# Kernel optimization log

Hardware: AMD Instinct MI355X
Metric: run time of the kernel (lower is better)

## Reference

```python
import jax, jax.numpy as jnp
import numpy as np

PH, PL = 2, 4          # high-band / low-band patch sizes
EPS_LN = 1e-5          # torch LayerNorm eps
EPS_COS = 1e-8         # torch F.cosine_similarity eps


def _ln(x, w, b):
    m = x.mean(-1, keepdims=True)
    v = ((x - m) ** 2).mean(-1, keepdims=True)
    return (x - m) / jnp.sqrt(v + EPS_LN) * w + b


def setup_inputs() -> dict:
    key = jax.random.key(0)
    ks = jax.random.split(key, 8)
    B, Cb, Cs, H, W = 16, 256, 512, 128, 128
    hid = int(Cb * 2.0)  # token_expansion = 2.0 -> 512

    def n(k, shape, s=0.02):
        return jax.random.normal(k, shape, jnp.float32) * s

    return {
        "x_big": jax.random.normal(ks[0], (B, Cb, H, W), jnp.float32),
        "x_small": jax.random.normal(ks[1], (B, Cs, H // 2, W // 2), jnp.float32),
        # hf MLP: Linear(Cb->hid), LayerNorm(hid), Linear(hid->Cb); weights stored (in,out)
        "hf_w1": n(ks[2], (Cb, hid)), "hf_b1": jnp.zeros((hid,), jnp.float32),
        "hf_ln_w": jnp.ones((hid,), jnp.float32), "hf_ln_b": jnp.zeros((hid,), jnp.float32),
        "hf_w2": n(ks[3], (hid, Cb)), "hf_b2": jnp.zeros((Cb,), jnp.float32),
        "hf_prompt": jax.random.normal(ks[4], (Cb,), jnp.float32),
        # low_proj: 1x1 conv dim_small -> dim_big
        "low_w": n(ks[5], (Cs, Cb)), "low_b": jnp.zeros((Cb,), jnp.float32),
        # lf gate MLP
        "lf_w1": n(ks[6], (Cb, hid)), "lf_b1": jnp.zeros((hid,), jnp.float32),
        "lf_ln_w": jnp.ones((hid,), jnp.float32), "lf_ln_b": jnp.zeros((hid,), jnp.float32),
        "lf_w2": n(ks[7], (hid, Cb)), "lf_b2": jnp.zeros((Cb,), jnp.float32),
    }


def reference(x_big, x_small, hf_w1, hf_b1, hf_ln_w, hf_ln_b, hf_w2, hf_b2,
              hf_prompt, low_w, low_b, lf_w1, lf_b1, lf_ln_w, lf_ln_b, lf_w2, lf_b2):
    B, C, H, W = x_big.shape
    h2, w2 = H // 2, W // 2

    # --- forward Haar (depthwise 2x2 stride-2 conv, /4), expressed as 2x2 pixel combos ---
    xr = x_big.reshape(B, C, h2, 2, w2, 2)
    p00, p01 = xr[:, :, :, 0, :, 0], xr[:, :, :, 0, :, 1]
    p10, p11 = xr[:, :, :, 1, :, 0], xr[:, :, :, 1, :, 1]
    a = (p00 + p01 + p10 + p11) * 0.25
    hb = (p00 - p01 + p10 - p11) * 0.25
    vb = (p00 + p01 - p10 - p11) * 0.25
    db = (p00 - p01 - p10 + p11) * 0.25

    # --- high-band enhancement: per-patch |mean| token -> MLP -> cosine gate ---
    def enhance_high(band):
        hh, ww = h2 // PH, w2 // PH
        bp = band.reshape(B, C, hh, PH, ww, PH)
        # tokens z: (B, hh*ww, C) = mean |patch|
        z = jnp.abs(bp).mean(axis=(3, 5)).transpose(0, 2, 3, 1).reshape(B, hh * ww, C)
        q = _ln(z @ hf_w1 + hf_b1, hf_ln_w, hf_ln_b) @ hf_w2 + hf_b2
        dot = q @ hf_prompt
        nq = jnp.linalg.norm(q, axis=-1)
        npr = jnp.linalg.norm(hf_prompt)
        sim = dot / (jnp.maximum(nq, EPS_COS) * jnp.maximum(npr, EPS_COS))
        alpha = jax.nn.relu(sim).reshape(B, 1, hh, 1, ww, 1)
        return (bp * alpha).reshape(B, C, h2, w2)

    h_enh = enhance_high(hb)
    v_enh = enhance_high(vb)
    d_enh = enhance_high(db)

    # --- low-band enhancement: 1x1 proj guide -> per-patch mean token -> sigmoid gate ---
    guide = jnp.einsum('bshw,sd->bdhw', x_small, low_w) + low_b[None, :, None, None]
    hh, ww = h2 // PL, w2 // PL
    k_tok = guide.reshape(B, C, hh, PL, ww, PL).mean(axis=(3, 5))
    k_tok = k_tok.transpose(0, 2, 3, 1).reshape(B, hh * ww, C)
    gate = jax.nn.sigmoid(_ln(k_tok @ lf_w1 + lf_b1, lf_ln_w, lf_ln_b) @ lf_w2 + lf_b2)
    gate = gate.reshape(B, hh, ww, C).transpose(0, 3, 1, 2)  # (B, C, hh, ww)
    a_enh = (a.reshape(B, C, hh, PL, ww, PL) * gate[:, :, :, None, :, None]).reshape(B, C, h2, w2)

    # --- inverse Haar (conv_transpose with raw weights, no /4) ---
    o00 = a_enh + h_enh + v_enh + d_enh
    o01 = a_enh - h_enh + v_enh - d_enh
    o10 = a_enh + h_enh - v_enh - d_enh
    o11 = a_enh - h_enh - v_enh + d_enh
    top = jnp.stack([o00, o01], axis=-1)           # (B,C,h2,w2,2)
    bot = jnp.stack([o10, o11], axis=-1)
    return jnp.stack([top, bot], axis=3).reshape(B, C, H, W)
```

## Files before the change

### kernel.cpp

```cpp
#include <hip/hip_runtime.h>
#include <cstdint>
#include <cmath>

typedef unsigned short u16;
typedef __bf16 bf16x8 __attribute__((ext_vector_type(8)));
typedef float f32x4 __attribute__((ext_vector_type(4)));

__device__ __forceinline__ u16 bf16_rne(float v) {
    union { float f; uint32_t u; } a; a.f = v;
    uint32_t r = a.u + 0x7fffu + ((a.u >> 16) & 1u);
    return (u16)(r >> 16);
}
__device__ __forceinline__ float bf16_to_f(u16 h) {
    union { uint32_t u; float f; } a; a.u = ((uint32_t)h) << 16;
    return a.f;
}
__device__ __forceinline__ uint32_t pack_pair(float v0, float v1, uint32_t& lopack) {
    const u16 h0 = bf16_rne(v0), h1 = bf16_rne(v1);
    const u16 l0 = bf16_rne(v0 - bf16_to_f(h0)), l1 = bf16_rne(v1 - bf16_to_f(h1));
    lopack = (uint32_t)l0 | ((uint32_t)l1 << 16);
    return (uint32_t)h0 | ((uint32_t)h1 << 16);
}


__device__ __forceinline__ void split_row(const float* __restrict__ src,
                                          u16* __restrict__ dh, u16* __restrict__ dl,
                                          int k, int ncol, int tidx)
{
    const int kt = k >> 5, kg = (k >> 3) & 3, e = k & 7;
    for (int col = tidx; col < ncol; col += 256) {
        const float v = src[(size_t)k * ncol + col];
        const u16 h  = bf16_rne(v);
        const u16 lo = bf16_rne(v - bf16_to_f(h));
        const size_t idx = ((size_t)((kt * 4 + kg) * ncol) + col) * 8 + e;
        dh[idx] = h; dl[idx] = lo;
    }
}

__global__ __launch_bounds__(256)
void k_front(const float* __restrict__ xb, const float* __restrict__ xs,
             const float* __restrict__ w1,  const float* __restrict__ w2,
             const float* __restrict__ low, const float* __restrict__ v1,
             const float* __restrict__ v2,
             float* __restrict__ z, float* __restrict__ sp,
             u16* __restrict__ w1fh,  u16* __restrict__ w1fl,
             u16* __restrict__ w2fh,  u16* __restrict__ w2fl,
             u16* __restrict__ lowfh, u16* __restrict__ lowfl,
             u16* __restrict__ v1fh,  u16* __restrict__ v1fl,
             u16* __restrict__ v2fh,  u16* __restrict__ v2fl)
{
    const int bid = blockIdx.x;
    if (bid < 4096) {
        const int bc  = bid;
        const int px  = threadIdx.x & 31;
        const int py0 = threadIdx.x >> 5;
        const float* base = xb + (size_t)bc * (128 * 128);
#pragma unroll
        for (int s = 0; s < 4; ++s) {
            const int py = py0 + 8 * s;
            const float* p = base + (4 * py) * 128 + 4 * px;
            const float4 r0 = *(const float4*)(p);
            const float4 r1 = *(const float4*)(p + 128);
            const float4 r2 = *(const float4*)(p + 256);
            const float4 r3 = *(const float4*)(p + 384);
            float zh = 0.f, zv = 0.f, zd = 0.f;
            {
                const float p00 = r0.x, p01 = r0.y, p10 = r1.x, p11 = r1.y;
                zh += fabsf(p00 - p01 + p10 - p11);
                zv += fabsf(p00 + p01 - p10 - p11);
                zd += fabsf(p00 - p01 - p10 + p11);
            }
            {
                const float p00 = r0.z, p01 = r0.w, p10 = r1.z, p11 = r1.w;
                zh += fabsf(p00 - p01 + p10 - p11);
                zv += fabsf(p00 + p01 - p10 - p11);
                zd += fabsf(p00 - p01 - p10 + p11);
            }
            {
                const float p00 = r2.x, p01 = r2.y, p10 = r3.x, p11 = r3.y;
                zh += fabsf(p00 - p01 + p10 - p11);
                zv += fabsf(p00 + p01 - p10 - p11);
                zd += fabsf(p00 - p01 - p10 + p11);
            }
            {
                const float p00 = r2.z, p01 = r2.w, p10 = r3.z, p11 = r3.w;
                zh += fabsf(p00 - p01 + p10 - p11);
                zv += fabsf(p00 + p01 - p10 - p11);
                zd += fabsf(p00 - p01 - p10 + p11);
            }
            const float sc = 0.0625f;
            const int t = py * 32 + px;
            z[(size_t)(0 * 4096 + bc) * 1024 + t] = zh * sc;
            z[(size_t)(1 * 4096 + bc) * 1024 + t] = zv * sc;
            z[(size_t)(2 * 4096 + bc) * 1024 + t] = zd * sc;
        }
    } else if (bid < 12288) {
        const int bs = bid - 4096;
        const int px = threadIdx.x & 15;
        const int py = threadIdx.x >> 4;
        const float* p = xs + (size_t)bs * 4096 + (4 * py) * 64 + 4 * px;
        float s = 0.f;
#pragma unroll
        for (int r = 0; r < 4; ++r) {
            const float4 v = *(const float4*)(p + 64 * r);
            s += v.x + v.y + v.z + v.w;
        }
        sp[(size_t)bs * 256 + threadIdx.x] = s * 0.0625f;
    } else {
        const int pb = bid - 12288;
        if      (pb < 256)  split_row(w1,  w1fh,  w1fl,  pb,        512, threadIdx.x);
        else if (pb < 768)  split_row(w2,  w2fh,  w2fl,  pb - 256,  256, threadIdx.x);
        else if (pb < 1280) split_row(low, lowfh, lowfl, pb - 768,  256, threadIdx.x);
        else if (pb < 1536) split_row(v1,  v1fh,  v1fl,  pb - 1280, 512, threadIdx.x);
        else                split_row(v2,  v2fh,  v2fl,  pb - 1536, 256, threadIdx.x);
    }
}

#define SWZ(t) (((t) & 7) << 3)

__global__ __launch_bounds__(256, 2)
void k_mlp(const float* __restrict__ z, const float* __restrict__ sp,
           const u16* __restrict__ w1fh, const u16* __restrict__ w1fl,
           const u16* __restrict__ w2fh, const u16* __restrict__ w2fl,
           const float* __restrict__ b1,
           const float* __restrict__ lnw, const float* __restrict__ lnb,
           const float* __restrict__ b2,
           const float* __restrict__ prompt,
           const u16* __restrict__ lowfh, const u16* __restrict__ lowfl,
           const float* __restrict__ lb_,
           const u16* __restrict__ v1fh, const u16* __restrict__ v1fl,
           const float* __restrict__ c1,
           const float* __restrict__ vlnw, const float* __restrict__ vlnb,
           const u16* __restrict__ v2fh, const u16* __restrict__ v2fl,
           const float* __restrict__ c2,
           float* __restrict__ alpha, float* __restrict__ gate)
{
    __shared__ uint32_t SM32[16384];
    __shared__ float partA[4][32], partB[4][32];
    __shared__ float partP[4];
    __shared__ float mu_s[32], rs_s[32];
    u16* SM = (u16*)SM32;

    const int tid = threadIdx.x;
    const int l   = tid & 63;
    const int w   = tid >> 6;
    const int lr  = l & 15;
    const int kg  = l >> 4;

    if (blockIdx.x >= 256) {
        const int hb   = blockIdx.x - 256;
        const int tile = hb & 31;
        const int bb   = hb >> 5;
        const int t0   = tile * 32;

        {
            const int c  = (tid & 127) * 2;
            const int th = (tid >> 7) * 16;
            const float* src0 = z + ((size_t)bb * 256 + c) * 1024 + t0 + th;
            const float* src1 = src0 + 1024;
#pragma unroll
            for (int j = 0; j < 16; j += 4) {
                const float4 v0 = *(const float4*)(src0 + j);
                const float4 v1 = *(const float4*)(src1 + j);
                const float a0[4] = {v0.x, v0.y, v0.z, v0.w};
                const float a1[4] = {v1.x, v1.y, v1.z, v1.w};
#pragma unroll
                for (int q = 0; q < 4; ++q) {
                    const int t = th + j + q;
                    uint32_t lp;
                    const uint32_t hp = pack_pair(a0[q], a1[q], lp);
                    const uint32_t idx32 = (uint32_t)(((t * 256 + c) ^ SWZ(t)) >> 1);
                    SM32[idx32]        = hp;
                    SM32[4096 + idx32] = lp;
                }
            }
        }
        __syncthreads();

        const int cb1 = w * 128 + lr;
        f32x4 acc[2][8];
#pragma unroll
        for (int m = 0; m < 2; ++m)
#pragma unroll
            for (int n = 0; n < 8; ++n) acc[m][n] = (f32x4){0.f, 0.f, 0.f, 0.f};

        for (int kt = 0; kt < 8; ++kt) {
            bf16x8 ah[2], al[2];
#pragma unroll
            for (int m = 0; m < 2; ++m) {
                const int idx = ((m * 16 + lr) * 256 + kt * 32 + kg * 8) ^ SWZ(lr);
                ah[m] = *(const bf16x8*)&SM[idx];
                al[m] = *(const bf16x8*)&SM[8192 + idx];
            }
            const size_t wb = ((size_t)((kt * 4 + kg) * 512) + cb1) * 8;
            bf16x8 bh[8], bl[8];
#pragma unroll
            for (int n = 0; n < 8; ++n) bh[n] = *(const bf16x8*)(w1fh + wb + n * 128);
#pragma unroll
            for (int n = 0; n < 8; ++n) bl[n] = *(const bf16x8*)(w1fl + wb + n * 128);
#pragma unroll
            for (int n = 0; n < 8; ++n)
#pragma unroll
                for (int m = 0; m < 2; ++m) acc[m][n] = __builtin_amdgcn_mfma_f32_16x16x32_bf16(ah[m], bh[n], acc[m][n], 0, 0, 0);
#pragma unroll
            for (int n = 0; n < 8; ++n)
#pragma unroll
                for (int m = 0; m < 2; ++m) acc[m][n] = __builtin_amdgcn_mfma_f32_16x16x32_bf16(ah[m], bl[n], acc[m][n], 0, 0, 0);
#pragma unroll
            for (int n = 0; n < 8; ++n)
#pragma unroll
                for (int m = 0; m < 2; ++m) acc[m][n] = __builtin_amdgcn_mfma_f32_16x16x32_bf16(al[m], bh[n], acc[m][n], 0, 0, 0);
        }

        float b1v[8];
#pragma unroll
        for (int n = 0; n < 8; ++n) b1v[n] = b1[cb1 + n * 16];
#pragma unroll
        for (int m = 0; m < 2; ++m)
#pragma unroll
            for (int n = 0; n < 8; ++n)
#pragma unroll
                for (int i = 0; i < 4; ++i) acc[m][n][i] += b1v[n];

#pragma unroll
        for (int m = 0; m < 2; ++m) {
            f32x4 s = (f32x4){0.f,0.f,0.f,0.f}, ss = (f32x4){0.f,0.f,0.f,0.f};
#pragma unroll
            for (int n = 0; n < 8; ++n)
#pragma unroll
                for (int i = 0; i < 4; ++i) { s[i] += acc[m][n][i]; ss[i] = fmaf(acc[m][n][i], acc[m][n][i], ss[i]); }
#pragma unroll
            for (int msk = 1; msk < 16; msk <<= 1) {
#pragma unroll
                for (int i = 0; i < 4; ++i) { s[i] += __shfl_xor(s[i], msk); ss[i] += __shfl_xor(ss[i], msk); }
            }
            if (lr == 0) {
#pragma unroll
                for (int i = 0; i < 4; ++i) {
                    partA[w][m * 16 + kg * 4 + i] = s[i];
                    partB[w][m * 16 + kg * 4 + i] = ss[i];
                }
            }
        }
        __syncthreads();
        if (tid < 32) {
            const float s  = partA[0][tid] + partA[1][tid] + partA[2][tid] + partA[3][tid];
            const float ss = partB[0][tid] + partB[1][tid] + partB[2][tid] + partB[3][tid];
            const float mu  = s * (1.f / 512.f);
            const float var = ss * (1.f / 512.f) - mu * mu;
            mu_s[tid] = mu;
            rs_s[tid] = rsqrtf(var + 1e-5f);
        }
        __syncthreads();

        {
            float lwv[8], lbv[8];
#pragma unroll
            for (int n = 0; n < 8; ++n) { lwv[n] = lnw[cb1 + n * 16]; lbv[n] = lnb[cb1 + n * 16]; }
#pragma unroll
            for (int m = 0; m < 2; ++m)
#pragma unroll
                for (int n = 0; n < 8; ++n)
#pragma unroll
                    for (int i = 0; i < 4; ++i) {
                        const int t = m * 16 + kg * 4 + i;
                        const float v = (acc[m][n][i] - mu_s[t]) * rs_s[t] * lwv[n] + lbv[n];
                        const u16 h  = bf16_rne(v);
                        const u16 lo = bf16_rne(v - bf16_to_f(h));
                        const int col = cb1 + n * 16;
                        const int idx = (t * 512 + col) ^ SWZ(t);
                        SM[idx] = h;
                        SM[16384 + idx] = lo;
                    }
        }
        __syncthreads();

        const int cb2 = w * 64 + lr;
        f32x4 acc2[2][4];
#pragma unroll
        for (int m = 0; m < 2; ++m)
#pragma unroll
            for (int n = 0; n < 4; ++n) acc2[m][n] = (f32x4){0.f, 0.f, 0.f, 0.f};

        for (int k2t = 0; k2t < 16; ++k2t) {
            bf16x8 ah[2], al[2];
#pragma unroll
            for (int m = 0; m < 2; ++m) {
                const int idx = ((m * 16 + lr) * 512 + k2t * 32 + kg * 8) ^ SWZ(lr);
                ah[m] = *(const bf16x8*)&SM[idx];
                al[m] = *(const bf16x8*)&SM[16384 + idx];
            }
            const size_t wb = ((size_t)((k2t * 4 + kg) * 256) + cb2) * 8;
            bf16x8 bh[4], bl[4];
#pragma unroll
            for (int n = 0; n < 4; ++n) bh[n] = *(const bf16x8*)(w2fh + wb + n * 128);
#pragma unroll
            for (int n = 0; n < 4; ++n) bl[n] = *(const bf16x8*)(w2fl + wb + n * 128);
#pragma unroll
            for (int n = 0; n < 4; ++n)
#pragma unroll
                for (int m = 0; m < 2; ++m) acc2[m][n] = __builtin_amdgcn_mfma_f32_16x16x32_bf16(ah[m], bh[n], acc2[m][n], 0, 0, 0);
#pragma unroll
            for (int n = 0; n < 4; ++n)
#pragma unroll
                for (int m = 0; m < 2; ++m) acc2[m][n] = __builtin_amdgcn_mfma_f32_16x16x32_bf16(ah[m], bl[n], acc2[m][n], 0, 0, 0);
#pragma unroll
            for (int n = 0; n < 4; ++n)
#pragma unroll
                for (int m = 0; m < 2; ++m) acc2[m][n] = __builtin_amdgcn_mfma_f32_16x16x32_bf16(al[m], bh[n], acc2[m][n], 0, 0, 0);
        }

        float b2v[4], prv[4];
#pragma unroll
        for (int n = 0; n < 4; ++n) { b2v[n] = b2[cb2 + n * 16]; prv[n] = prompt[cb2 + n * 16]; }
        {
            float pp = 0.f;
#pragma unroll
            for (int n = 0; n < 4; ++n) pp = fmaf(prv[n], prv[n], pp);
#pragma unroll
            for (int msk = 1; msk < 16; msk <<= 1) pp += __shfl_xor(pp, msk);
            if (l == 0) partP[w] = pp;
        }
#pragma unroll
        for (int m = 0; m < 2; ++m) {
            f32x4 dt = (f32x4){0.f,0.f,0.f,0.f}, nn = (f32x4){0.f,0.f,0.f,0.f};
#pragma unroll
            for (int n = 0; n < 4; ++n)
#pragma unroll
                for (int i = 0; i < 4; ++i) {
                    const float q = acc2[m][n][i] + b2v[n];
                    dt[i] = fmaf(q, prv[n], dt[i]);
                    nn[i] = fmaf(q, q, nn[i]);
                }
#pragma unroll
            for (int msk = 1; msk < 16; msk <<= 1) {
#pragma unroll
                for (int i = 0; i < 4; ++i) { dt[i] += __shfl_xor(dt[i], msk); nn[i] += __shfl_xor(nn[i], msk); }
            }
            if (lr == 0) {
#pragma unroll
                for (int i = 0; i < 4; ++i) {
                    partA[w][m * 16 + kg * 4 + i] = dt[i];
                    partB[w][m * 16 + kg * 4 + i] = nn[i];
                }
            }
        }
        __syncthreads();
        if (tid < 32) {
            const float dot = partA[0][tid] + partA[1][tid] + partA[2][tid] + partA[3][tid];
            const float nq2 = partB[0][tid] + partB[1][tid] + partB[2][tid] + partB[3][tid];
            const float ppt = partP[0] + partP[1] + partP[2] + partP[3];
            const float nq  = fmaxf(sqrtf(nq2), 1e-8f);
            const float npr = fmaxf(sqrtf(ppt), 1e-8f);
            alpha[(size_t)bb * 1024 + t0 + tid] = fmaxf(dot / (nq * npr), 0.f);
        }
    } else {
        const int tile = blockIdx.x & 15;
        const int b    = blockIdx.x >> 4;
        const int t0   = tile * 16;

        {
            const int s = tid * 2;
            const float* src0 = sp + ((size_t)b * 512 + s) * 256 + t0;
            const float* src1 = src0 + 256;
#pragma unroll
            for (int j = 0; j < 16; j += 4) {
                const float4 v0 = *(const float4*)(src0 + j);
                const float4 v1 = *(const float4*)(src1 + j);
                const float a0[4] = {v0.x, v0.y, v0.z, v0.w};
                const float a1[4] = {v1.x, v1.y, v1.z, v1.w};
#pragma unroll
                for (int q = 0; q < 4; ++q) {
                    const int t = j + q;
                    uint32_t lp;
                    const uint32_t hp = pack_pair(a0[q], a1[q], lp);
                    const uint32_t idx32 = (uint32_t)(((t * 512 + s) ^ SWZ(t)) >> 1);
                    SM32[idx32]        = hp;
                    SM32[4096 + idx32] = lp;
                }
            }
        }
        __syncthreads();

        const int cbA = w * 64 + lr;
        f32x4 accA[4];
#pragma unroll
        for (int n = 0; n < 4; ++n) accA[n] = (f32x4){0.f, 0.f, 0.f, 0.f};

        for (int kt = 0; kt < 16; ++kt) {
            const int idx = (lr * 512 + kt * 32 + kg * 8) ^ SWZ(lr);
            const bf16x8 ah = *(const bf16x8*)&SM[idx];
            const bf16x8 al = *(const bf16x8*)&SM[8192 + idx];
            const size_t wb = ((size_t)((kt * 4 + kg) * 256) + cbA) * 8;
            bf16x8 bh[4], bl[4];
#pragma unroll
            for (int n = 0; n < 4; ++n) bh[n] = *(const bf16x8*)(lowfh + wb + n * 128);
#pragma unroll
            for (int n = 0; n < 4; ++n) bl[n] = *(const bf16x8*)(lowfl + wb + n * 128);
#pragma unroll
            for (int n = 0; n < 4; ++n) accA[n] = __builtin_amdgcn_mfma_f32_16x16x32_bf16(ah, bh[n], accA[n], 0, 0, 0);
#pragma unroll
            for (int n = 0; n < 4; ++n) accA[n] = __builtin_amdgcn_mfma_f32_16x16x32_bf16(ah, bl[n], accA[n], 0, 0, 0);
#pragma unroll
            for (int n = 0; n < 4; ++n) accA[n] = __builtin_amdgcn_mfma_f32_16x16x32_bf16(al, bh[n], accA[n], 0, 0, 0);
        }
        __syncthreads();

        {
            float lbv[4];
#pragma unroll
            for (int n = 0; n < 4; ++n) lbv[n] = lb_[cbA + n * 16];
#pragma unroll
            for (int n = 0; n < 4; ++n)
#pragma unroll
                for (int i = 0; i < 4; ++i) {
                    const int t = kg * 4 + i;
                    const float v = accA[n][i] + lbv[n];
                    const u16 h  = bf16_rne(v);
                    const u16 lo = bf16_rne(v - bf16_to_f(h));
                    const int idx = (t * 256 + cbA + n * 16) ^ SWZ(t);
                    SM[idx] = h;
                    SM[4096 + idx] = lo;
                }
        }
        __syncthreads();

        const int cb1 = w * 128 + lr;
        f32x4 acc1[8];
#pragma unroll
        for (int n = 0; n < 8; ++n) acc1[n] = (f32x4){0.f, 0.f, 0.f, 0.f};

        for (int kt = 0; kt < 8; ++kt) {
            const int idx = (lr * 256 + kt * 32 + kg * 8) ^ SWZ(lr);
            const bf16x8 ah = *(const bf16x8*)&SM[idx];
            const bf16x8 al = *(const bf16x8*)&SM[4096 + idx];
            const size_t wb = ((size_t)((kt * 4 + kg) * 512) + cb1) * 8;
            bf16x8 bh[8], bl[8];
#pragma unroll
            for (int n = 0; n < 8; ++n) bh[n] = *(const bf16x8*)(v1fh + wb + n * 128);
#pragma unroll
            for (int n = 0; n < 8; ++n) bl[n] = *(const bf16x8*)(v1fl + wb + n * 128);
#pragma unroll
            for (int n = 0; n < 8; ++n) acc1[n] = __builtin_amdgcn_mfma_f32_16x16x32_bf16(ah, bh[n], acc1[n], 0, 0, 0);
#pragma unroll
            for (int n = 0; n < 8; ++n) acc1[n] = __builtin_amdgcn_mfma_f32_16x16x32_bf16(ah, bl[n], acc1[n], 0, 0, 0);
#pragma unroll
            for (int n = 0; n < 8; ++n) acc1[n] = __builtin_amdgcn_mfma_f32_16x16x32_bf16(al, bh[n], acc1[n], 0, 0, 0);
        }

        {
            float b1v[8];
#pragma unroll
            for (int n = 0; n < 8; ++n) b1v[n] = c1[cb1 + n * 16];
#pragma unroll
            for (int n = 0; n < 8; ++n)
#pragma unroll
                for (int i = 0; i < 4; ++i) acc1[n][i] += b1v[n];

            f32x4 s = (f32x4){0.f,0.f,0.f,0.f}, ss = (f32x4){0.f,0.f,0.f,0.f};
#pragma unroll
            for (int n = 0; n < 8; ++n)
#pragma unroll
                for (int i = 0; i < 4; ++i) { s[i] += acc1[n][i]; ss[i] = fmaf(acc1[n][i], acc1[n][i], ss[i]); }
#pragma unroll
            for (int msk = 1; msk < 16; msk <<= 1) {
#pragma unroll
                for (int i = 0; i < 4; ++i) { s[i] += __shfl_xor(s[i], msk); ss[i] += __shfl_xor(ss[i], msk); }
            }
            if (lr == 0) {
#pragma unroll
                for (int i = 0; i < 4; ++i) {
                    partA[w][kg * 4 + i] = s[i];
                    partB[w][kg * 4 + i] = ss[i];
                }
            }
        }
        __syncthreads();
        if (tid < 16) {
            const float s  = partA[0][tid] + partA[1][tid] + partA[2][tid] + partA[3][tid];
            const float ss = partB[0][tid] + partB[1][tid] + partB[2][tid] + partB[3][tid];
            const float mu  = s * (1.f / 512.f);
            const float var = ss * (1.f / 512.f) - mu * mu;
            mu_s[tid] = mu;
            rs_s[tid] = rsqrtf(var + 1e-5f);
        }
        __syncthreads();

        {
            float lwv[8], lbv[8];
#pragma unroll
            for (int n = 0; n < 8; ++n) { lwv[n] = vlnw[cb1 + n * 16]; lbv[n] = vlnb[cb1 + n * 16]; }
#pragma unroll
            for (int n = 0; n < 8; ++n)
#pragma unroll
                for (int i = 0; i < 4; ++i) {
                    const int t = kg * 4 + i;
                    const float v = (acc1[n][i] - mu_s[t]) * rs_s[t] * lwv[n] + lbv[n];
                    const u16 h  = bf16_rne(v);
                    const u16 lo = bf16_rne(v - bf16_to_f(h));
                    const int idx = (t * 512 + cb1 + n * 16) ^ SWZ(t);
                    SM[idx] = h;
                    SM[8192 + idx] = lo;
                }
        }
        __syncthreads();

        const int cb2 = w * 64 + lr;
        f32x4 acc2[4];
#pragma unroll
        for (int n = 0; n < 4; ++n) acc2[n] = (f32x4){0.f, 0.f, 0.f, 0.f};

        for (int k2t = 0; k2t < 16; ++k2t) {
            const int idx = (lr * 512 + k2t * 32 + kg * 8) ^ SWZ(lr);
            const bf16x8 ah = *(const bf16x8*)&SM[idx];
            const bf16x8 al = *(const bf16x8*)&SM[8192 + idx];
            const size_t wb = ((size_t)((k2t * 4 + kg) * 256) + cb2) * 8;
            bf16x8 bh[4], bl[4];
#pragma unroll
            for (int n = 0; n < 4; ++n) bh[n] = *(const bf16x8*)(v2fh + wb + n * 128);
#pragma unroll
            for (int n = 0; n < 4; ++n) bl[n] = *(const bf16x8*)(v2fl + wb + n * 128);
#pragma unroll
            for (int n = 0; n < 4; ++n) acc2[n] = __builtin_amdgcn_mfma_f32_16x16x32_bf16(ah, bh[n], acc2[n], 0, 0, 0);
#pragma unroll
            for (int n = 0; n < 4; ++n) acc2[n] = __builtin_amdgcn_mfma_f32_16x16x32_bf16(ah, bl[n], acc2[n], 0, 0, 0);
#pragma unroll
            for (int n = 0; n < 4; ++n) acc2[n] = __builtin_amdgcn_mfma_f32_16x16x32_bf16(al, bh[n], acc2[n], 0, 0, 0);
        }
        {
#pragma unroll
            for (int n = 0; n < 4; ++n) {
                const float b2v = c2[cb2 + n * 16];
                float4 o;
                o.x = 1.f / (1.f + expf(-(acc2[n][0] + b2v)));
                o.y = 1.f / (1.f + expf(-(acc2[n][1] + b2v)));
                o.z = 1.f / (1.f + expf(-(acc2[n][2] + b2v)));
                o.w = 1.f / (1.f + expf(-(acc2[n][3] + b2v)));
                *(float4*)&gate[((size_t)b * 256 + cb2 + n * 16) * 256 + t0 + kg * 4] = o;
            }
        }
    }
}

__global__ __launch_bounds__(256)
void k_final(const float* __restrict__ xb,
             const float* __restrict__ alpha,
             const float* __restrict__ gate,
             float* __restrict__ out)
{
    const int bc    = blockIdx.x >> 3;
    const int ytile = blockIdx.x & 7;
    const int x2 = threadIdx.x & 31;
    const int y  = ytile * 8 + (threadIdx.x >> 5);
    const int b  = bc >> 8;

    const float* p = xb + (size_t)bc * (128 * 128) + (2 * y) * 128 + 4 * x2;
    const float4 r0 = *(const float4*)(p);
    const float4 r1 = *(const float4*)(p + 128);

    const int th = (y >> 1) * 32 + x2;
    const float ah = alpha[(size_t)0 * 16384 + b * 1024 + th];
    const float av = alpha[(size_t)1 * 16384 + b * 1024 + th];
    const float ad = alpha[(size_t)2 * 16384 + b * 1024 + th];
    const float g  = gate[(size_t)bc * 256 + (y >> 2) * 16 + (x2 >> 1)];

    float4 o_top, o_bot;
    {
        const float p00 = r0.x, p01 = r0.y, p10 = r1.x, p11 = r1.y;
        const float a  = 0.25f * (p00 + p01 + p10 + p11) * g;
        const float hb = 0.25f * (p00 - p01 + p10 - p11) * ah;
        const float vb = 0.25f * (p00 + p01 - p10 - p11) * av;
        const float db = 0.25f * (p00 - p01 - p10 + p11) * ad;
        o_top.x = a + hb + vb + db;  o_top.y = a - hb + vb - db;
        o_bot.x = a + hb - vb - db;  o_bot.y = a - hb - vb + db;
    }
    {
        const float p00 = r0.z, p01 = r0.w, p10 = r1.z, p11 = r1.w;
        const float a  = 0.25f * (p00 + p01 + p10 + p11) * g;
        const float hb = 0.25f * (p00 - p01 + p10 - p11) * ah;
        const float vb = 0.25f * (p00 + p01 - p10 - p11) * av;
        const float db = 0.25f * (p00 - p01 - p10 + p11) * ad;
        o_top.z = a + hb + vb + db;  o_top.w = a - hb + vb - db;
        o_bot.z = a + hb - vb - db;  o_bot.w = a - hb - vb + db;
    }
    float* q = out + (size_t)bc * (128 * 128) + (2 * y) * 128 + 4 * x2;
    *(float4*)(q)       = o_top;
    *(float4*)(q + 128) = o_bot;
}

extern "C" void kernel_launch(void* const* d_in, const int* in_sizes, int n_in,
                              void* d_out, int out_size, void* d_ws, size_t ws_size,
                              hipStream_t stream)
{
    (void)in_sizes; (void)n_in; (void)out_size; (void)ws_size;
    const float* x_big     = (const float*)d_in[0];
    const float* x_small   = (const float*)d_in[1];
    const float* hf_w1     = (const float*)d_in[2];
    const float* hf_b1     = (const float*)d_in[3];
    const float* hf_ln_w   = (const float*)d_in[4];
    const float* hf_ln_b   = (const float*)d_in[5];
    const float* hf_w2     = (const float*)d_in[6];
    const float* hf_b2     = (const float*)d_in[7];
    const float* hf_prompt = (const float*)d_in[8];
    const float* low_w     = (const float*)d_in[9];
    const float* low_b     = (const float*)d_in[10];
    const float* lf_w1     = (const float*)d_in[11];
    const float* lf_b1     = (const float*)d_in[12];
    const float* lf_ln_w   = (const float*)d_in[13];
    const float* lf_ln_b   = (const float*)d_in[14];
    const float* lf_w2     = (const float*)d_in[15];
    const float* lf_b2     = (const float*)d_in[16];
    float* out = (float*)d_out;

    float* ws    = (float*)d_ws;
    float* z     = ws;
    float* sp    = z + (size_t)3 * 4096 * 1024;
    float* alpha = sp + (size_t)16 * 512 * 256;
    float* gate  = alpha + (size_t)3 * 16 * 1024;
    u16* w1fh  = (u16*)(gate + (size_t)16 * 256 * 256);
    u16* w1fl  = w1fh  + 131072;
    u16* w2fh  = w1fl  + 131072;
    u16* w2fl  = w2fh  + 131072;
    u16* lowfh = w2fl  + 131072;
    u16* lowfl = lowfh + 131072;
    u16* lw1fh = lowfl + 131072;
    u16* lw1fl = lw1fh + 131072;
    u16* lw2fh = lw1fl + 131072;
    u16* lw2fl = lw2fh + 131072;

    k_front<<<14336, 256, 0, stream>>>(x_big, x_small,
                                       hf_w1, hf_w2, low_w, lf_w1, lf_w2,
                                       z, sp,
                                       w1fh, w1fl, w2fh, w2fl,
                                       lowfh, lowfl, lw1fh, lw1fl, lw2fh, lw2fl);
    k_mlp  <<<1792, 256, 0, stream>>>(z, sp,
                                      w1fh, w1fl, w2fh, w2fl,
                                      hf_b1, hf_ln_w, hf_ln_b, hf_b2, hf_prompt,
                                      lowfh, lowfl, low_b,
                                      lw1fh, lw1fl, lf_b1, lf_ln_w, lf_ln_b,
                                      lw2fh, lw2fl, lf_b2,
                                      alpha, gate);
    k_final<<<32768, 256, 0, stream>>>(x_big, alpha, gate, out);
}
```

Measured before the change: 712.5 us.

## Double token tile per block in MLP kernel to halve weight refetches

The fused MLP kernel now runs 512-thread blocks, each handling twice as many tokens: 64 per high-band tile and 32 per low-band tile. Each wave covers more M rows and fewer N columns, so every weight fragment loaded from global memory feeds more MFMAs. The aim is to cut the redundant weight traffic across the split-bf16 GEMMs. In exchange, shared memory per block doubles to about 128KB+, which may limit occupancy, and the grid shrinks to 896 blocks.

```diff
diff --git a/kernel.cpp b/kernel.cpp
--- a/kernel.cpp
+++ b/kernel.cpp
@@ -118,7 +118,7 @@
 
 #define SWZ(t) (((t) & 7) << 3)
 
-__global__ __launch_bounds__(256, 2)
+__global__ __launch_bounds__(512, 2)
 void k_mlp(const float* __restrict__ z, const float* __restrict__ sp,
            const u16* __restrict__ w1fh, const u16* __restrict__ w1fl,
            const u16* __restrict__ w2fh, const u16* __restrict__ w2fl,
@@ -135,10 +135,10 @@
            const float* __restrict__ c2,
            float* __restrict__ alpha, float* __restrict__ gate)
 {
-    __shared__ uint32_t SM32[16384];
-    __shared__ float partA[4][32], partB[4][32];
-    __shared__ float partP[4];
-    __shared__ float mu_s[32], rs_s[32];
+    __shared__ uint32_t SM32[32768];
+    __shared__ float partA[8][64], partB[8][64];
+    __shared__ float partP[8];
+    __shared__ float mu_s[64], rs_s[64];
     u16* SM = (u16*)SM32;
 
     const int tid = threadIdx.x;
@@ -147,11 +147,11 @@
     const int lr  = l & 15;
     const int kg  = l >> 4;
 
-    if (blockIdx.x >= 256) {
-        const int hb   = blockIdx.x - 256;
-        const int tile = hb & 31;
-        const int bb   = hb >> 5;
-        const int t0   = tile * 32;
+    if (blockIdx.x >= 128) {
+        const int hb   = blockIdx.x - 128;
+        const int tile = hb & 15;
+        const int bb   = hb >> 4;
+        const int t0   = tile * 64;
 
         {
             const int c  = (tid & 127) * 2;
@@ -171,62 +171,62 @@
                     const uint32_t hp = pack_pair(a0[q], a1[q], lp);
                     const uint32_t idx32 = (uint32_t)(((t * 256 + c) ^ SWZ(t)) >> 1);
                     SM32[idx32]        = hp;
-                    SM32[4096 + idx32] = lp;
-                }
-            }
-        }
-        __syncthreads();
-
-        const int cb1 = w * 128 + lr;
-        f32x4 acc[2][8];
-#pragma unroll
-        for (int m = 0; m < 2; ++m)
-#pragma unroll
-            for (int n = 0; n < 8; ++n) acc[m][n] = (f32x4){0.f, 0.f, 0.f, 0.f};
+                    SM32[8192 + idx32] = lp;
+                }
+            }
+        }
+        __syncthreads();
+
+        const int cb1 = w * 64 + lr;
+        f32x4 acc[4][4];
+#pragma unroll
+        for (int m = 0; m < 4; ++m)
+#pragma unroll
+            for (int n = 0; n < 4; ++n) acc[m][n] = (f32x4){0.f, 0.f, 0.f, 0.f};
 
         for (int kt = 0; kt < 8; ++kt) {
-            bf16x8 ah[2], al[2];
-#pragma unroll
-            for (int m = 0; m < 2; ++m) {
+            bf16x8 ah[4], al[4];
+#pragma unroll
+            for (int m = 0; m < 4; ++m) {
                 const int idx = ((m * 16 + lr) * 256 + kt * 32 + kg * 8) ^ SWZ(lr);
                 ah[m] = *(const bf16x8*)&SM[idx];
-                al[m] = *(const bf16x8*)&SM[8192 + idx];
+                al[m] = *(const bf16x8*)&SM[16384 + idx];
             }
             const size_t wb = ((size_t)((kt * 4 + kg) * 512) + cb1) * 8;
-            bf16x8 bh[8], bl[8];
-#pragma unroll
-            for (int n = 0; n < 8; ++n) bh[n] = *(const bf16x8*)(w1fh + wb + n * 128);
-#pragma unroll
-            for (int n = 0; n < 8; ++n) bl[n] = *(const bf16x8*)(w1fl + wb + n * 128);
-#pragma unroll
-            for (int n = 0; n < 8; ++n)
-#pragma unroll
-                for (int m = 0; m < 2; ++m) acc[m][n] = __builtin_amdgcn_mfma_f32_16x16x32_bf16(ah[m], bh[n], acc[m][n], 0, 0, 0);
-#pragma unroll
-            for (int n = 0; n < 8; ++n)
-#pragma unroll
-                for (int m = 0; m < 2; ++m) acc[m][n] = __builtin_amdgcn_mfma_f32_16x16x32_bf16(ah[m], bl[n], acc[m][n], 0, 0, 0);
-#pragma unroll
-            for (int n = 0; n < 8; ++n)
-#pragma unroll
-                for (int m = 0; m < 2; ++m) acc[m][n] = __builtin_amdgcn_mfma_f32_16x16x32_bf16(al[m], bh[n], acc[m][n], 0, 0, 0);
-        }
-
-        float b1v[8];
-#pragma unroll
-        for (int n = 0; n < 8; ++n) b1v[n] = b1[cb1 + n * 16];
-#pragma unroll
-        for (int m = 0; m < 2; ++m)
-#pragma unroll
-            for (int n = 0; n < 8; ++n)
+            bf16x8 bh[4], bl[4];
+#pragma unroll
+            for (int n = 0; n < 4; ++n) bh[n] = *(const bf16x8*)(w1fh + wb + n * 128);
+#pragma unroll
+            for (int n = 0; n < 4; ++n) bl[n] = *(const bf16x8*)(w1fl + wb + n * 128);
+#pragma unroll
+            for (int n = 0; n < 4; ++n)
+#pragma unroll
+                for (int m = 0; m < 4; ++m) acc[m][n] = __builtin_amdgcn_mfma_f32_16x16x32_bf16(ah[m], bh[n], acc[m][n], 0, 0, 0);
+#pragma unroll
+            for (int n = 0; n < 4; ++n)
+#pragma unroll
+                for (int m = 0; m < 4; ++m) acc[m][n] = __builtin_amdgcn_mfma_f32_16x16x32_bf16(ah[m], bl[n], acc[m][n], 0, 0, 0);
+#pragma unroll
+            for (int n = 0; n < 4; ++n)
+#pragma unroll
+                for (int m = 0; m < 4; ++m) acc[m][n] = __builtin_amdgcn_mfma_f32_16x16x32_bf16(al[m], bh[n], acc[m][n], 0, 0, 0);
+        }
+
+        float b1v[4];
+#pragma unroll
+        for (int n = 0; n < 4; ++n) b1v[n] = b1[cb1 + n * 16];
+#pragma unroll
+        for (int m = 0; m < 4; ++m)
+#pragma unroll
+            for (int n = 0; n < 4; ++n)
 #pragma unroll
                 for (int i = 0; i < 4; ++i) acc[m][n][i] += b1v[n];
 
 #pragma unroll
-        for (int m = 0; m < 2; ++m) {
+        for (int m = 0; m < 4; ++m) {
             f32x4 s = (f32x4){0.f,0.f,0.f,0.f}, ss = (f32x4){0.f,0.f,0.f,0.f};
 #pragma unroll
-            for (int n = 0; n < 8; ++n)
+            for (int n = 0; n < 4; ++n)
 #pragma unroll
                 for (int i = 0; i < 4; ++i) { s[i] += acc[m][n][i]; ss[i] = fmaf(acc[m][n][i], acc[m][n][i], ss[i]); }
 #pragma unroll
@@ -243,9 +243,10 @@
             }
         }
         __syncthreads();
-        if (tid < 32) {
-            const float s  = partA[0][tid] + partA[1][tid] + partA[2][tid] + partA[3][tid];
-            const float ss = partB[0][tid] + partB[1][tid] + partB[2][tid] + partB[3][tid];
+        if (tid < 64) {
+            float s = 0.f, ss = 0.f;
+#pragma unroll
+            for (int ww = 0; ww < 8; ++ww) { s += partA[ww][tid]; ss += partB[ww][tid]; }
             const float mu  = s * (1.f / 512.f);
             const float var = ss * (1.f / 512.f) - mu * mu;
             mu_s[tid] = mu;
@@ -254,13 +255,13 @@
         __syncthreads();
 
         {
-            float lwv[8], lbv[8];
-#pragma unroll
-            for (int n = 0; n < 8; ++n) { lwv[n] = lnw[cb1 + n * 16]; lbv[n] = lnb[cb1 + n * 16]; }
-#pragma unroll
-            for (int m = 0; m < 2; ++m)
-#pragma unroll
-                for (int n = 0; n < 8; ++n)
+            float lwv[4], lbv[4];
+#pragma unroll
+            for (int n = 0; n < 4; ++n) { lwv[n] = lnw[cb1 + n * 16]; lbv[n] = lnb[cb1 + n * 16]; }
+#pragma unroll
+            for (int m = 0; m < 4; ++m)
+#pragma unroll
+                for (int n = 0; n < 4; ++n)
 #pragma unroll
                     for (int i = 0; i < 4; ++i) {
                         const int t = m * 16 + kg * 4 + i;
@@ -270,62 +271,62 @@
                         const int col = cb1 + n * 16;
                         const int idx = (t * 512 + col) ^ SWZ(t);
                         SM[idx] = h;
-                        SM[16384 + idx] = lo;
+                        SM[32768 + idx] = lo;
                     }
         }
         __syncthreads();
 
-        const int cb2 = w * 64 + lr;
-        f32x4 acc2[2][4];
-#pragma unroll
-        for (int m = 0; m < 2; ++m)
-#pragma unroll
-            for (int n = 0; n < 4; ++n) acc2[m][n] = (f32x4){0.f, 0.f, 0.f, 0.f};
+        const int cb2 = w * 32 + lr;
+        f32x4 acc2[4][2];
+#pragma unroll
+        for (int m = 0; m < 4; ++m)
+#pragma unroll
+            for (int n = 0; n < 2; ++n) acc2[m][n] = (f32x4){0.f, 0.f, 0.f, 0.f};
 
         for (int k2t = 0; k2t < 16; ++k2t) {
-            bf16x8 ah[2], al[2];
-#pragma unroll
-            for (int m = 0; m < 2; ++m) {
+            bf16x8 ah[4], al[4];
+#pragma unroll
+            for (int m = 0; m < 4; ++m) {
                 const int idx = ((m * 16 + lr) * 512 + k2t * 32 + kg * 8) ^ SWZ(lr);
                 ah[m] = *(const bf16x8*)&SM[idx];
-                al[m] = *(const bf16x8*)&SM[16384 + idx];
+                al[m] = *(const bf16x8*)&SM[32768 + idx];
             }
             const size_t wb = ((size_t)((k2t * 4 + kg) * 256) + cb2) * 8;
-            bf16x8 bh[4], bl[4];
-#pragma unroll
-            for (int n = 0; n < 4; ++n) bh[n] = *(const bf16x8*)(w2fh + wb + n * 128);
-#pragma unroll
-            for (int n = 0; n < 4; ++n) bl[n] = *(const bf16x8*)(w2fl + wb + n * 128);
-#pragma unroll
-            for (int n = 0; n < 4; ++n)
-#pragma unroll
-                for (int m = 0; m < 2; ++m) acc2[m][n] = __builtin_amdgcn_mfma_f32_16x16x32_bf16(ah[m], bh[n], acc2[m][n], 0, 0, 0);
-#pragma unroll
-            for (int n = 0; n < 4; ++n)
-#pragma unroll
-                for (int m = 0; m < 2; ++m) acc2[m][n] = __builtin_amdgcn_mfma_f32_16x16x32_bf16(ah[m], bl[n], acc2[m][n], 0, 0, 0);
-#pragma unroll
-            for (int n = 0; n < 4; ++n)
-#pragma unroll
-                for (int m = 0; m < 2; ++m) acc2[m][n] = __builtin_amdgcn_mfma_f32_16x16x32_bf16(al[m], bh[n], acc2[m][n], 0, 0, 0);
-        }
-
-        float b2v[4], prv[4];
-#pragma unroll
-        for (int n = 0; n < 4; ++n) { b2v[n] = b2[cb2 + n * 16]; prv[n] = prompt[cb2 + n * 16]; }
+            bf16x8 bh[2], bl[2];
+#pragma unroll
+            for (int n = 0; n < 2; ++n) bh[n] = *(const bf16x8*)(w2fh + wb + n * 128);
+#pragma unroll
+            for (int n = 0; n < 2; ++n) bl[n] = *(const bf16x8*)(w2fl + wb + n * 128);
+#pragma unroll
+            for (int n = 0; n < 2; ++n)
+#pragma unroll
+                for (int m = 0; m < 4; ++m) acc2[m][n] = __builtin_amdgcn_mfma_f32_16x16x32_bf16(ah[m], bh[n], acc2[m][n], 0, 0, 0);
+#pragma unroll
+            for (int n = 0; n < 2; ++n)
+#pragma unroll
+                for (int m = 0; m < 4; ++m) acc2[m][n] = __builtin_amdgcn_mfma_f32_16x16x32_bf16(ah[m], bl[n], acc2[m][n], 0, 0, 0);
+#pragma unroll
+            for (int n = 0; n < 2; ++n)
+#pragma unroll
+                for (int m = 0; m < 4; ++m) acc2[m][n] = __builtin_amdgcn_mfma_f32_16x16x32_bf16(al[m], bh[n], acc2[m][n], 0, 0, 0);
+        }
+
+        float b2v[2], prv[2];
+#pragma unroll
+        for (int n = 0; n < 2; ++n) { b2v[n] = b2[cb2 + n * 16]; prv[n] = prompt[cb2 + n * 16]; }
         {
             float pp = 0.f;
 #pragma unroll
-            for (int n = 0; n < 4; ++n) pp = fmaf(prv[n], prv[n], pp);
+            for (int n = 0; n < 2; ++n) pp = fmaf(prv[n], prv[n], pp);
 #pragma unroll
             for (int msk = 1; msk < 16; msk <<= 1) pp += __shfl_xor(pp, msk);
             if (l == 0) partP[w] = pp;
         }
 #pragma unroll
-        for (int m = 0; m < 2; ++m) {
+        for (int m = 0; m < 4; ++m) {
             f32x4 dt = (f32x4){0.f,0.f,0.f,0.f}, nn = (f32x4){0.f,0.f,0.f,0.f};
 #pragma unroll
-            for (int n = 0; n < 4; ++n)
+            for (int n = 0; n < 2; ++n)
 #pragma unroll
                 for (int i = 0; i < 4; ++i) {
                     const float q = acc2[m][n][i] + b2v[n];
@@ -346,22 +347,23 @@
             }
         }
         __syncthreads();
-        if (tid < 32) {
-            const float dot = partA[0][tid] + partA[1][tid] + partA[2][tid] + partA[3][tid];
-            const float nq2 = partB[0][tid] + partB[1][tid] + partB[2][tid] + partB[3][tid];
-            const float ppt = partP[0] + partP[1] + partP[2] + partP[3];
+        if (tid < 64) {
+            float dot = 0.f, nq2 = 0.f, ppt = 0.f;
+#pragma unroll
+            for (int ww = 0; ww < 8; ++ww) { dot += partA[ww][tid]; nq2 += partB[ww][tid]; ppt += partP[ww]; }
             const float nq  = fmaxf(sqrtf(nq2), 1e-8f);
             const float npr = fmaxf(sqrtf(ppt), 1e-8f);
             alpha[(size_t)bb * 1024 + t0 + tid] = fmaxf(dot / (nq * npr), 0.f);
         }
     } else {
-        const int tile = blockIdx.x & 15;
-        const int b    = blockIdx.x >> 4;
-        const int t0   = tile * 16;
-
-        {
-            const int s = tid * 2;
-            const float* src0 = sp + ((size_t)b * 512 + s) * 256 + t0;
+        const int tile = blockIdx.x & 7;
+        const int b    = blockIdx.x >> 3;
+        const int t0   = tile * 32;
+
+        {
+            const int s  = (tid & 255) * 2;
+            const int th = (tid >> 8) * 16;
+            const float* src0 = sp + ((size_t)b * 512 + s) * 256 + t0 + th;
             const float* src1 = src0 + 256;
 #pragma unroll
             for (int j = 0; j < 16; j += 4) {
@@ -371,114 +373,146 @@
                 const float a1[4] = {v1.x, v1.y, v1.z, v1.w};
 #pragma unroll
                 for (int q = 0; q < 4; ++q) {
-                    const int t = j + q;
+                    const int t = th + j + q;
                     uint32_t lp;
                     const uint32_t hp = pack_pair(a0[q], a1[q], lp);
                     const uint32_t idx32 = (uint32_t)(((t * 512 + s) ^ SWZ(t)) >> 1);
                     SM32[idx32]        = hp;
-                    SM32[4096 + idx32] = lp;
-                }
-            }
-        }
-        __syncthreads();
-
-        const int cbA = w * 64 + lr;
-        f32x4 accA[4];
-#pragma unroll
-        for (int n = 0; n < 4; ++n) accA[n] = (f32x4){0.f, 0.f, 0.f, 0.f};
+                    SM32[8192 + idx32] = lp;
+                }
+            }
+        }
+        __syncthreads();
+
+        const int cbA = w * 32 + lr;
+        f32x4 accA[2][2];
+#pragma unroll
+        for (int m = 0; m < 2; ++m)
+#pragma unroll
+            for (int n = 0; n < 2; ++n) accA[m][n] = (f32x4){0.f, 0.f, 0.f, 0.f};
 
         for (int kt = 0; kt < 16; ++kt) {
-            const int idx = (lr * 512 + kt * 32 + kg * 8) ^ SWZ(lr);
-            const bf16x8 ah = *(const bf16x8*)&SM[idx];
-            const bf16x8 al = *(const bf16x8*)&SM[8192 + idx];
+            bf16x8 ah[2], al[2];
+#pragma unroll
+            for (int m = 0; m < 2; ++m) {
+                const int idx = ((m * 16 + lr) * 512 + kt * 32 + kg * 8) ^ SWZ(lr);
+                ah[m] = *(const bf16x8*)&SM[idx];
+                al[m] = *(const bf16x8*)&SM[16384 + idx];
+            }
             const size_t wb = ((size_t)((kt * 4 + kg) * 256) + cbA) * 8;
+            bf16x8 bh[2], bl[2];
+#pragma unroll
+            for (int n = 0; n < 2; ++n) bh[n] = *(const bf16x8*)(lowfh + wb + n * 128);
+#pragma unroll
+            for (int n = 0; n < 2; ++n) bl[n] = *(const bf16x8*)(lowfl + wb + n * 128);
+#pragma unroll
+            for (int n = 0; n < 2; ++n)
+#pragma unroll
+                for (int m = 0; m < 2; ++m) accA[m][n] = __builtin_amdgcn_mfma_f32_16x16x32_bf16(ah[m], bh[n], accA[m][n], 0, 0, 0);
+#pragma unroll
+            for (int n = 0; n < 2; ++n)
+#pragma unroll
+                for (int m = 0; m < 2; ++m) accA[m][n] = __builtin_amdgcn_mfma_f32_16x16x32_bf16(ah[m], bl[n], accA[m][n], 0, 0, 0);
+#pragma unroll
+            for (int n = 0; n < 2; ++n)
+#pragma unroll
+                for (int m = 0; m < 2; ++m) accA[m][n] = __builtin_amdgcn_mfma_f32_16x16x32_bf16(al[m], bh[n], accA[m][n], 0, 0, 0);
+        }
+        __syncthreads();
+
+        {
+            float lbv[2];
+#pragma unroll
+            for (int n = 0; n < 2; ++n) lbv[n] = lb_[cbA + n * 16];
+#pragma unroll
+            for (int m = 0; m < 2; ++m)
+#pragma unroll
+                for (int n = 0; n < 2; ++n)
+#pragma unroll
+                    for (int i = 0; i < 4; ++i) {
+                        const int t = m * 16 + kg * 4 + i;
+                        const float v = accA[m][n][i] + lbv[n];
+                        const u16 h  = bf16_rne(v);
+                        const u16 lo = bf16_rne(v - bf16_to_f(h));
+                        const int idx = (t * 256 + cbA + n * 16) ^ SWZ(t);
+                        SM[32768 + idx] = h;
+                        SM[40960 + idx] = lo;
+                    }
+        }
+        __syncthreads();
+
+        const int cb1 = w * 64 + lr;
+        f32x4 acc1[2][4];
+#pragma unroll
+        for (int m = 0; m < 2; ++m)
+#pragma unroll
+            for (int n = 0; n < 4; ++n) acc1[m][n] = (f32x4){0.f, 0.f, 0.f, 0.f};
+
+        for (int kt = 0; kt < 8; ++kt) {
+            bf16x8 ah[2], al[2];
+#pragma unroll
+            for (int m = 0; m < 2; ++m) {
+                const int idx = ((m * 16 + lr) * 256 + kt * 32 + kg * 8) ^ SWZ(lr);
+                ah[m] = *(const bf16x8*)&SM[32768 + idx];
+                al[m] = *(const bf16x8*)&SM[40960 + idx];
+            }
+            const size_t wb = ((size_t)((kt * 4 + kg) * 512) + cb1) * 8;
             bf16x8 bh[4], bl[4];
 #pragma unroll
-            for (int n = 0; n < 4; ++n) bh[n] = *(const bf16x8*)(lowfh + wb + n * 128);
-#pragma unroll
-            for (int n = 0; n < 4; ++n) bl[n] = *(const bf16x8*)(lowfl + wb + n * 128);
-#pragma unroll
-            for (int n = 0; n < 4; ++n) accA[n] = __builtin_amdgcn_mfma_f32_16x16x32_bf16(ah, bh[n], accA[n], 0, 0, 0);
-#pragma unroll
-            for (int n = 0; n < 4; ++n) accA[n] = __builtin_amdgcn_mfma_f32_16x16x32_bf16(ah, bl[n], accA[n], 0, 0, 0);
-#pragma unroll
-            for (int n = 0; n < 4; ++n) accA[n] = __builtin_amdgcn_mfma_f32_16x16x32_bf16(al, bh[n], accA[n], 0, 0, 0);
-        }
-        __syncthreads();
-
-        {
-            float lbv[4];
-#pragma unroll
-            for (int n = 0; n < 4; ++n) lbv[n] = lb_[cbA + n * 16];
-#pragma unroll
-            for (int n = 0; n < 4; ++n)
-#pragma unroll
-                for (int i = 0; i < 4; ++i) {
-                    const int t = kg * 4 + i;
-                    const float v = accA[n][i] + lbv[n];
-                    const u16 h  = bf16_rne(v);
-                    const u16 lo = bf16_rne(v - bf16_to_f(h));
-                    const int idx = (t * 256 + cbA + n * 16) ^ SWZ(t);
-                    SM[idx] = h;
-                    SM[4096 + idx] = lo;
-                }
-        }
-        __syncthreads();
-
-        const int cb1 = w * 128 + lr;
-        f32x4 acc1[8];
-#pragma unroll
-        for (int n = 0; n < 8; ++n) acc1[n] = (f32x4){0.f, 0.f, 0.f, 0.f};
-
-        for (int kt = 0; kt < 8; ++kt) {
-            const int idx = (lr * 256 + kt * 32 + kg * 8) ^ SWZ(lr);
-            const bf16x8 ah = *(const bf16x8*)&SM[idx];
-            const bf16x8 al = *(const bf16x8*)&SM[4096 + idx];
-            const size_t wb = ((size_t)((kt * 4 + kg) * 512) + cb1) * 8;
-            bf16x8 bh[8], bl[8];
-#pragma unroll
-            for (int n = 0; n < 8; ++n) bh[n] = *(const bf16x8*)(v1fh + wb + n * 128);
-#pragma unroll
-            for (int n = 0; n < 8; ++n) bl[n] = *(const bf16x8*)(v1fl + wb + n * 128);
-#pragma unroll
-            for (int n = 0; n < 8; ++n) acc1[n] = __builtin_amdgcn_mfma_f32_16x16x32_bf16(ah, bh[n], acc1[n], 0, 0, 0);
-#pragma unroll
-            for (int n = 0; n < 8; ++n) acc1[n] = __builtin_amdgcn_mfma_f32_16x16x32_bf16(ah, bl[n], acc1[n], 0, 0, 0);
-#pragma unroll
-            for (int n = 0; n < 8; ++n) acc1[n] = __builtin_amdgcn_mfma_f32_16x16x32_bf16(al, bh[n], acc1[n], 0, 0, 0);
-        }
-
-        {
-            float b1v[8];
-#pragma unroll
-            for (int n = 0; n < 8; ++n) b1v[n] = c1[cb1 + n * 16];
-#pragma unroll
-            for (int n = 0; n < 8; ++n)
-#pragma unroll
-                for (int i = 0; i < 4; ++i) acc1[n][i] += b1v[n];
-
-            f32x4 s = (f32x4){0.f,0.f,0.f,0.f}, ss = (f32x4){0.f,0.f,0.f,0.f};
-#pragma unroll
-            for (int n = 0; n < 8; ++n)
-#pragma unroll
-                for (int i = 0; i < 4; ++i) { s[i] += acc1[n][i]; ss[i] = fmaf(acc1[n][i], acc1[n][i], ss[i]); }
-#pragma unroll
-            for (int msk = 1; msk < 16; msk <<= 1) {
-#pragma unroll
-                for (int i = 0; i < 4; ++i) { s[i] += __shfl_xor(s[i], msk); ss[i] += __shfl_xor(ss[i], msk); }
-            }
-            if (lr == 0) {
-#pragma unroll
-                for (int i = 0; i < 4; ++i) {
-                    partA[w][kg * 4 + i] = s[i];
-                    partB[w][kg * 4 + i] = ss[i];
-                }
-            }
-        }
-        __syncthreads();
-        if (tid < 16) {
-            const float s  = partA[0][tid] + partA[1][tid] + partA[2][tid] + partA[3][tid];
-            const float ss = partB[0][tid] + partB[1][tid] + partB[2][tid] + partB[3][tid];
+            for (int n = 0; n < 4; ++n) bh[n] = *(const bf16x8*)(v1fh + wb + n * 128);
+#pragma unroll
+            for (int n = 0; n < 4; ++n) bl[n] = *(const bf16x8*)(v1fl + wb + n * 128);
+#pragma unroll
+            for (int n = 0; n < 4; ++n)
+#pragma unroll
+                for (int m = 0; m < 2; ++m) acc1[m][n] = __builtin_amdgcn_mfma_f32_16x16x32_bf16(ah[m], bh[n], acc1[m][n], 0, 0, 0);
+#pragma unroll
+            for (int n = 0; n < 4; ++n)
+#pragma unroll
+                for (int m = 0; m < 2; ++m) acc1[m][n] = __builtin_amdgcn_mfma_f32_16x16x32_bf16(ah[m], bl[n], acc1[m][n], 0, 0, 0);
+#pragma unroll
+            for (int n = 0; n < 4; ++n)
+#pragma unroll
+                for (int m = 0; m < 2; ++m) acc1[m][n] = __builtin_amdgcn_mfma_f32_16x16x32_bf16(al[m], bh[n], acc1[m][n], 0, 0, 0);
+        }
+
+        {
+            float b1v[4];
+#pragma unroll
+            for (int n = 0; n < 4; ++n) b1v[n] = c1[cb1 + n * 16];
+#pragma unroll
+            for (int m = 0; m < 2; ++m)
+#pragma unroll
+                for (int n = 0; n < 4; ++n)
+#pragma unroll
+                    for (int i = 0; i < 4; ++i) acc1[m][n][i] += b1v[n];
+
+#pragma unroll
+            for (int m = 0; m < 2; ++m) {
+                f32x4 s = (f32x4){0.f,0.f,0.f,0.f}, ss = (f32x4){0.f,0.f,0.f,0.f};
+#pragma unroll
+                for (int n = 0; n < 4; ++n)
+#pragma unroll
+                    for (int i = 0; i < 4; ++i) { s[i] += acc1[m][n][i]; ss[i] = fmaf(acc1[m][n][i], acc1[m][n][i], ss[i]); }
+#pragma unroll
+                for (int msk = 1; msk < 16; msk <<= 1) {
+#pragma unroll
+                    for (int i = 0; i < 4; ++i) { s[i] += __shfl_xor(s[i], msk); ss[i] += __shfl_xor(ss[i], msk); }
+                }
+                if (lr == 0) {
+#pragma unroll
+                    for (int i = 0; i < 4; ++i) {
+                        partA[w][m * 16 + kg * 4 + i] = s[i];
+                        partB[w][m * 16 + kg * 4 + i] = ss[i];
+                    }
+                }
+            }
+        }
+        __syncthreads();
+        if (tid < 32) {
+            float s = 0.f, ss = 0.f;
+#pragma unroll
+            for (int ww = 0; ww < 8; ++ww) { s += partA[ww][tid]; ss += partB[ww][tid]; }
             const float mu  = s * (1.f / 512.f);
             const float var = ss * (1.f / 512.f) - mu * mu;
             mu_s[tid] = mu;
@@ -487,57 +521,73 @@
         __syncthreads();
 
         {
-            float lwv[8], lbv[8];
-#pragma unroll
-            for (int n = 0; n < 8; ++n) { lwv[n] = vlnw[cb1 + n * 16]; lbv[n] = vlnb[cb1 + n * 16]; }
-#pragma unroll
-            for (int n = 0; n < 8; ++n)
-#pragma unroll
-                for (int i = 0; i < 4; ++i) {
-                    const int t = kg * 4 + i;
-                    const float v = (acc1[n][i] - mu_s[t]) * rs_s[t] * lwv[n] + lbv[n];
-                    const u16 h  = bf16_rne(v);
-                    const u16 lo = bf16_rne(v - bf16_to_f(h));
-                    const int idx = (t * 512 + cb1 + n * 16) ^ SWZ(t);
-                    SM[idx] = h;
-                    SM[8192 + idx] = lo;
-                }
-        }
-        __syncthreads();
-
-        const int cb2 = w * 64 + lr;
-        f32x4 acc2[4];
-#pragma unroll
-        for (int n = 0; n < 4; ++n) acc2[n] = (f32x4){0.f, 0.f, 0.f, 0.f};
+            float lwv[4], lbv[4];
+#pragma unroll
+            for (int n = 0; n < 4; ++n) { lwv[n] = vlnw[cb1 + n * 16]; lbv[n] = vlnb[cb1 + n * 16]; }
+#pragma unroll
+            for (int m = 0; m < 2; ++m)
+#pragma unroll
+                for (int n = 0; n < 4; ++n)
+#pragma unroll
+                    for (int i = 0; i < 4; ++i) {
+                        const int t = m * 16 + kg * 4 + i;
+                        const float v = (acc1[m][n][i] - mu_s[t]) * rs_s[t] * lwv[n] + lbv[n];
+                        const u16 h  = bf16_rne(v);
+                        const u16 lo = bf16_rne(v - bf16_to_f(h));
+                        const int idx = (t * 512 + cb1 + n * 16) ^ SWZ(t);
+                        SM[idx] = h;
+                        SM[16384 + idx] = lo;
+                    }
+        }
+        __syncthreads();
+
+        const int cb2 = w * 32 + lr;
+        f32x4 acc2[2][2];
+#pragma unroll
+        for (int m = 0; m < 2; ++m)
+#pragma unroll
+            for (int n = 0; n < 2; ++n) acc2[m][n] = (f32x4){0.f, 0.f, 0.f, 0.f};
 
         for (int k2t = 0; k2t < 16; ++k2t) {
-            const int idx = (lr * 512 + k2t * 32 + kg * 8) ^ SWZ(lr);
-            const bf16x8 ah = *(const bf16x8*)&SM[idx];
-            const bf16x8 al = *(const bf16x8*)&SM[8192 + idx];
+            bf16x8 ah[2], al[2];
+#pragma unroll
+            for (int m = 0; m < 2; ++m) {
+                const int idx = ((m * 16 + lr) * 512 + k2t * 32 + kg * 8) ^ SWZ(lr);
+                ah[m] = *(const bf16x8*)&SM[idx];
+                al[m] = *(const bf16x8*)&SM[16384 + idx];
+            }
             const size_t wb = ((size_t)((k2t * 4 + kg) * 256) + cb2) * 8;
-            bf16x8 bh[4], bl[4];
-#pragma unroll
-            for (int n = 0; n < 4; ++n) bh[n] = *(const bf16x8*)(v2fh + wb + n * 128);
-#pragma unroll
-            for (int n = 0; n < 4; ++n) bl[n] = *(const bf16x8*)(v2fl + wb + n * 128);
-#pragma unroll
-            for (int n = 0; n < 4; ++n) acc2[n] = __builtin_amdgcn_mfma_f32_16x16x32_bf16(ah, bh[n], acc2[n], 0, 0, 0);
-#pragma unroll
-            for (int n = 0; n < 4; ++n) acc2[n] = __builtin_amdgcn_mfma_f32_16x16x32_bf16(ah, bl[n], acc2[n], 0, 0, 0);
-#pragma unroll
-            for (int n = 0; n < 4; ++n) acc2[n] = __builtin_amdgcn_mfma_f32_16x16x32_bf16(al, bh[n], acc2[n], 0, 0, 0);
-        }
-        {
-#pragma unroll
-            for (int n = 0; n < 4; ++n) {
-                const float b2v = c2[cb2 + n * 16];
-                float4 o;
-                o.x = 1.f / (1.f + expf(-(acc2[n][0] + b2v)));
-                o.y = 1.f / (1.f + expf(-(acc2[n][1] + b2v)));
-                o.z = 1.f / (1.f + expf(-(acc2[n][2] + b2v)));
-                o.w = 1.f / (1.f + expf(-(acc2[n][3] + b2v)));
-                *(float4*)&gate[((size_t)b * 256 + cb2 + n * 16) * 256 + t0 + kg * 4] = o;
-            }
+            bf16x8 bh[2], bl[2];
+#pragma unroll
+            for (int n = 0; n < 2; ++n) bh[n] = *(const bf16x8*)(v2fh + wb + n * 128);
+#pragma unroll
+            for (int n = 0; n < 2; ++n) bl[n] = *(const bf16x8*)(v2fl + wb + n * 128);
+#pragma unroll
+            for (int n = 0; n < 2; ++n)
+#pragma unroll
+                for (int m = 0; m < 2; ++m) acc2[m][n] = __builtin_amdgcn_mfma_f32_16x16x32_bf16(ah[m], bh[n], acc2[m][n], 0, 0, 0);
+#pragma unroll
+            for (int n = 0; n < 2; ++n)
+#pragma unroll
+                for (int m = 0; m < 2; ++m) acc2[m][n] = __builtin_amdgcn_mfma_f32_16x16x32_bf16(ah[m], bl[n], acc2[m][n], 0, 0, 0);
+#pragma unroll
+            for (int n = 0; n < 2; ++n)
+#pragma unroll
+                for (int m = 0; m < 2; ++m) acc2[m][n] = __builtin_amdgcn_mfma_f32_16x16x32_bf16(al[m], bh[n], acc2[m][n], 0, 0, 0);
+        }
+        {
+#pragma unroll
+            for (int m = 0; m < 2; ++m)
+#pragma unroll
+                for (int n = 0; n < 2; ++n) {
+                    const float b2v = c2[cb2 + n * 16];
+                    float4 o;
+                    o.x = 1.f / (1.f + expf(-(acc2[m][n][0] + b2v)));
+                    o.y = 1.f / (1.f + expf(-(acc2[m][n][1] + b2v)));
+                    o.z = 1.f / (1.f + expf(-(acc2[m][n][2] + b2v)));
+                    o.w = 1.f / (1.f + expf(-(acc2[m][n][3] + b2v)));
+                    *(float4*)&gate[((size_t)b * 256 + cb2 + n * 16) * 256 + t0 + m * 16 + kg * 4] = o;
+                }
         }
     }
 }
@@ -633,12 +683,12 @@
                                        z, sp,
                                        w1fh, w1fl, w2fh, w2fl,
                                        lowfh, lowfl, lw1fh, lw1fl, lw2fh, lw2fl);
-    k_mlp  <<<1792, 256, 0, stream>>>(z, sp,
-                                      w1fh, w1fl, w2fh, w2fl,
-                                      hf_b1, hf_ln_w, hf_ln_b, hf_b2, hf_prompt,
-                                      lowfh, lowfl, low_b,
-                                      lw1fh, lw1fl, lf_b1, lf_ln_w, lf_ln_b,
-                                      lw2fh, lw2fl, lf_b2,
-                                      alpha, gate);
+    k_mlp  <<<896, 512, 0, stream>>>(z, sp,
+                                     w1fh, w1fl, w2fh, w2fl,
+                                     hf_b1, hf_ln_w, hf_ln_b, hf_b2, hf_prompt,
+                                     lowfh, lowfl, low_b,
+                                     lw1fh, lw1fl, lf_b1, lf_ln_w, lf_ln_b,
+                                     lw2fh, lw2fl, lf_b2,
+                                     alpha, gate);
     k_final<<<32768, 256, 0, stream>>>(x_big, alpha, gate, out);
 }
```

Measured after the change: 714.3 us. No clear change (+0.3%).
